# Kernel optimization log

Measured on AMD Instinct MI355X. Metric: run time of the kernel, lower is better.

## Reference

```python
import jax, jax.numpy as jnp
import numpy as np

D_EMB, D_PROJ, N_HEADS, HIDDEN = 640, 256, 4, 128
HEAD_DIM = D_PROJ // N_HEADS
B = 65536
EPS = 1e-5


def setup_inputs() -> dict:
    key = jax.random.key(0)
    ks = jax.random.split(key, 14)
    def w(k, shape, fan_in):
        return (jax.random.normal(k, shape, jnp.float32) / np.sqrt(fan_in)).astype(jnp.float32)
    return {
        "global_diff": jax.random.normal(ks[0], (B, D_EMB), jnp.float32),
        "local_diff": jax.random.normal(ks[1], (B, D_EMB), jnp.float32),
        # global/local projections ([in, out] layout; math identical to torch Linear)
        "Wg": w(ks[2], (D_EMB, D_PROJ), D_EMB), "bg": jnp.zeros((D_PROJ,), jnp.float32),
        "Wl": w(ks[3], (D_EMB, D_PROJ), D_EMB), "bl": jnp.zeros((D_PROJ,), jnp.float32),
        # MultiheadAttention packed in-proj (q|k|v) and out-proj
        "W_in": w(ks[4], (D_PROJ, 3 * D_PROJ), D_PROJ), "b_in": jnp.zeros((3 * D_PROJ,), jnp.float32),
        "W_out": w(ks[5], (D_PROJ, D_PROJ), D_PROJ), "b_out": jnp.zeros((D_PROJ,), jnp.float32),
        # LayerNorm
        "gamma": jnp.ones((D_PROJ,), jnp.float32), "beta": jnp.zeros((D_PROJ,), jnp.float32),
        # MLP head
        "W1": w(ks[6], (D_PROJ, HIDDEN), D_PROJ), "b1": jnp.zeros((HIDDEN,), jnp.float32),
        "W2": w(ks[7], (HIDDEN, 1), HIDDEN), "b2": jnp.zeros((1,), jnp.float32),
    }


def reference(global_diff, local_diff, Wg, bg, Wl, bl, W_in, b_in, W_out, b_out,
              gamma, beta, W1, b1, W2, b2):
    # projections (eval mode: dropout inactive)
    g = global_diff @ Wg + bg              # [B, P] -- the single query token
    l = local_diff @ Wl + bl               # [B, P]
    kv = jnp.stack([g, l], axis=1)         # [B, 2, P]

    Wq, Wk, Wv = jnp.split(W_in, 3, axis=1)
    bq, bk, bv = jnp.split(b_in, 3)
    b = g.shape[0]
    q = (g @ Wq + bq).reshape(b, N_HEADS, HEAD_DIM)        # [B, H, d]
    k = (kv @ Wk + bk).reshape(b, 2, N_HEADS, HEAD_DIM)    # [B, 2, H, d]
    v = (kv @ Wv + bv).reshape(b, 2, N_HEADS, HEAD_DIM)

    scale = 1.0 / np.sqrt(HEAD_DIM)
    scores = jnp.einsum('bhd,bshd->bhs', q, k) * scale     # [B, H, 2]
    attn = jax.nn.softmax(scores, axis=-1)
    ctx = jnp.einsum('bhs,bshd->bhd', attn, v).reshape(b, D_PROJ)
    attended = ctx @ W_out + b_out                         # [B, P]

    # residual + LayerNorm (eps=1e-5, torch default)
    x = g + attended
    mu = jnp.mean(x, axis=-1, keepdims=True)
    var = jnp.mean(jnp.square(x - mu), axis=-1, keepdims=True)
    y = (x - mu) * jax.lax.rsqrt(var + EPS) * gamma + beta

    # MLP head: Linear -> exact GELU (torch default) -> Linear
    h = jax.nn.gelu(y @ W1 + b1, approximate=False)
    out = (h @ W2 + b2).squeeze(-1)                        # [B]
    return out
```

## Files before the change

### kernel.cpp

```cpp
#include <hip/hip_runtime.h>
#include <math.h>

typedef __attribute__((ext_vector_type(4))) float f32x4;
typedef __attribute__((ext_vector_type(8))) __bf16 bf16x8;

static constexpr int WG_OFF = 0;
static constexpr int WL_OFF = 163840;
static constexpr int WQ_OFF = 327680;
static constexpr int WK_OFF = 393216;
static constexpr int WV_OFF = 458752;
static constexpr int WO_OFF = 524288;
static constexpr int W1_OFF = 589824;
static constexpr int W_TOTAL = 622592;

__device__ __forceinline__ unsigned short f2bf(float f) {
  unsigned u = __builtin_bit_cast(unsigned, f);
  u += 0x7FFFu + ((u >> 16) & 1u);
  return (unsigned short)(u >> 16);
}

__device__ __forceinline__ f32x4 mfma16(bf16x8 a, bf16x8 b, f32x4 c) {
  return __builtin_amdgcn_mfma_f32_16x16x32_bf16(a, b, c, 0, 0, 0);
}
__device__ __forceinline__ f32x4 fzero4() {
  f32x4 v; v[0] = 0.f; v[1] = 0.f; v[2] = 0.f; v[3] = 0.f; return v;
}

__device__ __forceinline__ bf16x8 ldB(const unsigned short* __restrict__ ws, int fragIdx, int lane) {
  return *(const bf16x8*)(ws + (size_t)(fragIdx * 64 + lane) * 8);
}

template <int STRIDE>
__device__ __forceinline__ bf16x8 ldA(const char* s, int row, int kbyte) {
  return *(const bf16x8*)(s + row * STRIDE + (kbyte ^ ((row & 7) << 4)));
}

__device__ __forceinline__ bf16x8 cvt8(float4 a, float4 b) {
  bf16x8 t;
  t[0] = (__bf16)a.x; t[1] = (__bf16)a.y; t[2] = (__bf16)a.z; t[3] = (__bf16)a.w;
  t[4] = (__bf16)b.x; t[5] = (__bf16)b.y; t[6] = (__bf16)b.z; t[7] = (__bf16)b.w;
  return t;
}

template <int N>
__device__ __forceinline__ void red16(float* v) {
#pragma unroll
  for (int m = 1; m < 16; m <<= 1) {
#pragma unroll
    for (int i = 0; i < N; ++i) v[i] += __shfl_xor(v[i], m);
  }
}

__device__ __forceinline__ void stageA32(const float* __restrict__ A, char* sA, int tid) {
#pragma unroll
  for (int i = 0; i < 5; ++i) {
    const int idx = i * 512 + tid;
    const int row = idx / 80;
    const int c8 = idx - row * 80;
    const float* ap = A + (size_t)idx * 8;
    float4 f0 = *(const float4*)ap;
    float4 f1 = *(const float4*)(ap + 4);
    *(bf16x8*)(sA + row * 1280 + ((c8 * 16) ^ ((row & 7) << 4))) = cvt8(f0, f1);
  }
}

__device__ __forceinline__ void proj640(const char* sA, const unsigned short* __restrict__ wsW,
                                        const float* __restrict__ bias, char* sDst,
                                        int f0, int lane) {
  const int l15 = lane & 15, kg4 = lane >> 4;
  f32x4 acc[2][2];
#pragma unroll
  for (int m = 0; m < 2; ++m)
#pragma unroll
    for (int n = 0; n < 2; ++n) acc[m][n] = fzero4();
  bf16x8 bp[4][2];
#pragma unroll
  for (int p = 0; p < 4; ++p) {
    bp[p][0] = ldB(wsW, p * 16 + f0, lane);
    bp[p][1] = ldB(wsW, p * 16 + f0 + 1, lane);
  }
#pragma unroll
  for (int kt = 0; kt < 20; ++kt) {
    bf16x8 b0 = bp[kt & 3][0], b1 = bp[kt & 3][1];
    if (kt < 16) {
      bp[kt & 3][0] = ldB(wsW, (kt + 4) * 16 + f0, lane);
      bp[kt & 3][1] = ldB(wsW, (kt + 4) * 16 + f0 + 1, lane);
    }
    const int kb = kt * 64 + kg4 * 16;
#pragma unroll
    for (int m = 0; m < 2; ++m) {
      bf16x8 a = ldA<1280>(sA, m * 16 + l15, kb);
      acc[m][0] = mfma16(a, b0, acc[m][0]);
      acc[m][1] = mfma16(a, b1, acc[m][1]);
    }
  }
#pragma unroll
  for (int n = 0; n < 2; ++n) {
    const int col = (f0 + n) * 16 + l15;
    const float bv = bias[col];
#pragma unroll
    for (int m = 0; m < 2; ++m)
#pragma unroll
      for (int r = 0; r < 4; ++r) {
        const int row = m * 16 + kg4 * 4 + r;
        *(__bf16*)(sDst + row * 512 + ((col * 2) ^ ((row & 7) << 4))) =
            (__bf16)(acc[m][n][r] + bv);
      }
  }
}

__device__ __forceinline__ void gemm256(const char* sA, const unsigned short* __restrict__ wsW,
                                        int f0, f32x4 (&acc)[2][2], int lane) {
  const int l15 = lane & 15, kg4 = lane >> 4;
#pragma unroll
  for (int kt = 0; kt < 8; ++kt) {
    bf16x8 b0 = ldB(wsW, kt * 16 + f0, lane);
    bf16x8 b1 = ldB(wsW, kt * 16 + f0 + 1, lane);
    const int kb = kt * 64 + kg4 * 16;
#pragma unroll
    for (int m = 0; m < 2; ++m) {
      bf16x8 a = ldA<512>(sA, m * 16 + l15, kb);
      acc[m][0] = mfma16(a, b0, acc[m][0]);
      acc[m][1] = mfma16(a, b1, acc[m][1]);
    }
  }
}

__device__ __forceinline__ void gemm256d(const char* sG, const char* sL,
                                         const unsigned short* __restrict__ wsW, int f0,
                                         f32x4 (&ag)[2][2], f32x4 (&al)[2][2], int lane) {
  const int l15 = lane & 15, kg4 = lane >> 4;
#pragma unroll
  for (int kt = 0; kt < 8; ++kt) {
    bf16x8 b0 = ldB(wsW, kt * 16 + f0, lane);
    bf16x8 b1 = ldB(wsW, kt * 16 + f0 + 1, lane);
    const int kb = kt * 64 + kg4 * 16;
#pragma unroll
    for (int m = 0; m < 2; ++m) {
      bf16x8 g = ldA<512>(sG, m * 16 + l15, kb);
      bf16x8 l = ldA<512>(sL, m * 16 + l15, kb);
      ag[m][0] = mfma16(g, b0, ag[m][0]);
      ag[m][1] = mfma16(g, b1, ag[m][1]);
      al[m][0] = mfma16(l, b0, al[m][0]);
      al[m][1] = mfma16(l, b1, al[m][1]);
    }
  }
}

__global__ void convert_w(const float* __restrict__ Wg, const float* __restrict__ Wl,
                          const float* __restrict__ Win, const float* __restrict__ Wout,
                          const float* __restrict__ W1, unsigned short* __restrict__ ws) {
  const int tid = blockIdx.x * 256 + threadIdx.x;
  if (tid >= W_TOTAL) return;
  const float* src;
  int stride, coloff, base, lognf;
  if (tid < WL_OFF)      { src = Wg;   stride = 256; coloff = 0;   base = WG_OFF; lognf = 4; }
  else if (tid < WQ_OFF) { src = Wl;   stride = 256; coloff = 0;   base = WL_OFF; lognf = 4; }
  else if (tid < WK_OFF) { src = Win;  stride = 768; coloff = 0;   base = WQ_OFF; lognf = 4; }
  else if (tid < WV_OFF) { src = Win;  stride = 768; coloff = 256; base = WK_OFF; lognf = 4; }
  else if (tid < WO_OFF) { src = Win;  stride = 768; coloff = 512; base = WV_OFF; lognf = 4; }
  else if (tid < W1_OFF) { src = Wout; stride = 256; coloff = 0;   base = WO_OFF; lognf = 4; }
  else                   { src = W1;   stride = 128; coloff = 0;   base = W1_OFF; lognf = 3; }
  const int idx = tid - base;
  const int j = idx & 7;
  const int lane = (idx >> 3) & 63;
  const int fl = idx >> 9;
  const int n = fl & ((1 << lognf) - 1);
  const int kt = fl >> lognf;
  const int k = kt * 32 + (lane >> 4) * 8 + j;
  const int col = coloff + n * 16 + (lane & 15);
  ws[tid] = f2bf(src[k * stride + col]);
}

__global__ __launch_bounds__(512, 4) void dca_fused(
    const float* __restrict__ gdiff, const float* __restrict__ ldiff,
    const float* __restrict__ bg, const float* __restrict__ bl,
    const float* __restrict__ bin, const float* __restrict__ bout,
    const float* __restrict__ gamma, const float* __restrict__ beta,
    const float* __restrict__ b1, const float* __restrict__ W2,
    const float* __restrict__ b2, const unsigned short* __restrict__ wsw,
    float* __restrict__ out) {
  __shared__ __align__(16) char sMem[73728];
  char* sA = sMem;
  char* sG = sMem + 40960;
  char* sL = sMem + 57344;
  float* sSc = (float*)sMem;
  float* sLN = (float*)(sMem + 2048);
  float* sMu = (float*)(sMem + 4096);
  float* sPO = (float*)(sMem + 4352);
  char* sY = sMem + 8192;

  const int tid = threadIdx.x;
  const int blk = blockIdx.x;
  const int lane = tid & 63, l15 = lane & 15, kg4 = lane >> 4;
  const int w = tid >> 6;
  const int f0 = w * 2;

  stageA32(gdiff + (size_t)blk * 32 * 640, sA, tid);
  __syncthreads();
  proj640(sA, wsw + WG_OFF, bg, sG, f0, lane);
  __syncthreads();
  stageA32(ldiff + (size_t)blk * 32 * 640, sA, tid);
  __syncthreads();
  proj640(sA, wsw + WL_OFF, bl, sL, f0, lane);
  __syncthreads();

  f32x4 q[2][2];
#pragma unroll
  for (int m = 0; m < 2; ++m)
#pragma unroll
    for (int n = 0; n < 2; ++n) q[m][n] = fzero4();
  gemm256(sG, wsw + WQ_OFF, f0, q, lane);
#pragma unroll
  for (int n = 0; n < 2; ++n) {
    const float bv = bin[(f0 + n) * 16 + l15];
#pragma unroll
    for (int m = 0; m < 2; ++m)
#pragma unroll
      for (int r = 0; r < 4; ++r) q[m][n][r] += bv;
  }
  f32x4 kg[2][2], kl[2][2];
#pragma unroll
  for (int m = 0; m < 2; ++m)
#pragma unroll
    for (int n = 0; n < 2; ++n) { kg[m][n] = fzero4(); kl[m][n] = fzero4(); }
  gemm256d(sG, sL, wsw + WK_OFF, f0, kg, kl, lane);

  float s[16];
#pragma unroll
  for (int m = 0; m < 2; ++m)
#pragma unroll
    for (int r = 0; r < 4; ++r) {
      float t0 = 0.f, t1 = 0.f;
#pragma unroll
      for (int n = 0; n < 2; ++n) {
        t0 += q[m][n][r] * kg[m][n][r];
        t1 += q[m][n][r] * kl[m][n][r];
      }
      s[m * 4 + r] = t0;
      s[8 + m * 4 + r] = t1;
    }
  red16<16>(s);
  if (l15 < 2) {
#pragma unroll
    for (int r = 0; r < 4; ++r) {
      const int row = l15 * 16 + kg4 * 4 + r;
      sSc[(w * 32 + row) * 2 + 0] = s[l15 * 4 + r];
      sSc[(w * 32 + row) * 2 + 1] = s[8 + l15 * 4 + r];
    }
  }
  __syncthreads();
  float a0[2][4], a1[2][4];
  {
    const int pw = w ^ 1;
#pragma unroll
    for (int m = 0; m < 2; ++m)
#pragma unroll
      for (int r = 0; r < 4; ++r) {
        const int row = m * 16 + kg4 * 4 + r;
        const float t0 = s[m * 4 + r] + sSc[(pw * 32 + row) * 2 + 0];
        const float t1 = s[8 + m * 4 + r] + sSc[(pw * 32 + row) * 2 + 1];
        const float d = (t0 - t1) * 0.125f;
        const float t = 1.0f / (1.0f + expf(d));
        a1[m][r] = t;
        a0[m][r] = 1.0f - t;
      }
  }
  f32x4 vg[2][2], vl[2][2];
#pragma unroll
  for (int m = 0; m < 2; ++m)
#pragma unroll
    for (int n = 0; n < 2; ++n) { vg[m][n] = fzero4(); vl[m][n] = fzero4(); }
  gemm256d(sG, sL, wsw + WV_OFF, f0, vg, vl, lane);
  f32x4 ctx[2][2];
#pragma unroll
  for (int n = 0; n < 2; ++n) {
    const float bv = bin[512 + (f0 + n) * 16 + l15];
#pragma unroll
    for (int m = 0; m < 2; ++m)
#pragma unroll
      for (int r = 0; r < 4; ++r)
        ctx[m][n][r] = a0[m][r] * vg[m][n][r] + a1[m][r] * vl[m][n][r] + bv;
  }
  __syncthreads();
#pragma unroll
  for (int n = 0; n < 2; ++n) {
    const int col = (f0 + n) * 16 + l15;
#pragma unroll
    for (int m = 0; m < 2; ++m)
#pragma unroll
      for (int r = 0; r < 4; ++r) {
        const int row = m * 16 + kg4 * 4 + r;
        *(__bf16*)(sL + row * 512 + ((col * 2) ^ ((row & 7) << 4))) = (__bf16)ctx[m][n][r];
      }
  }
  __syncthreads();

  f32x4 at[2][2];
#pragma unroll
  for (int m = 0; m < 2; ++m)
#pragma unroll
    for (int n = 0; n < 2; ++n) at[m][n] = fzero4();
  gemm256(sL, wsw + WO_OFF, f0, at, lane);
  float st[16];
#pragma unroll
  for (int i = 0; i < 16; ++i) st[i] = 0.f;
#pragma unroll
  for (int n = 0; n < 2; ++n) {
    const int col = (f0 + n) * 16 + l15;
    const float bv = bout[col];
#pragma unroll
    for (int m = 0; m < 2; ++m)
#pragma unroll
      for (int r = 0; r < 4; ++r) {
        const int row = m * 16 + kg4 * 4 + r;
        const float g =
            (float)*(const __bf16*)(sG + row * 512 + ((col * 2) ^ ((row & 7) << 4)));
        const float x = at[m][n][r] + bv + g;
        at[m][n][r] = x;
        st[m * 4 + r] += x;
        st[8 + m * 4 + r] += x * x;
      }
  }
  red16<16>(st);
  if (l15 < 2) {
#pragma unroll
    for (int r = 0; r < 4; ++r) {
      const int row = l15 * 16 + kg4 * 4 + r;
      sLN[(w * 32 + row) * 2 + 0] = st[l15 * 4 + r];
      sLN[(w * 32 + row) * 2 + 1] = st[8 + l15 * 4 + r];
    }
  }
  __syncthreads();
  if (tid < 64) {
    const int row = tid >> 1, j = tid & 1;
    float v = 0.f;
#pragma unroll
    for (int ww = 0; ww < 8; ++ww) v += sLN[(ww * 32 + row) * 2 + j];
    sMu[row * 2 + j] = v;
  }
  __syncthreads();
  float mu[2][4], rs[2][4];
#pragma unroll
  for (int m = 0; m < 2; ++m)
#pragma unroll
    for (int r = 0; r < 4; ++r) {
      const int row = m * 16 + kg4 * 4 + r;
      const float m_ = sMu[row * 2 + 0] * (1.0f / 256.0f);
      const float var = sMu[row * 2 + 1] * (1.0f / 256.0f) - m_ * m_;
      mu[m][r] = m_;
      rs[m][r] = rsqrtf(var + 1e-5f);
    }
#pragma unroll
  for (int n = 0; n < 2; ++n) {
    const int col = (f0 + n) * 16 + l15;
    const float ga = gamma[col], be = beta[col];
#pragma unroll
    for (int m = 0; m < 2; ++m)
#pragma unroll
      for (int r = 0; r < 4; ++r) {
        const int row = m * 16 + kg4 * 4 + r;
        const float y = (at[m][n][r] - mu[m][r]) * rs[m][r] * ga + be;
        *(__bf16*)(sY + row * 512 + ((col * 2) ^ ((row & 7) << 4))) = (__bf16)y;
      }
  }
  __syncthreads();

  f32x4 ha[2];
  ha[0] = fzero4();
  ha[1] = fzero4();
#pragma unroll
  for (int kt = 0; kt < 8; ++kt) {
    bf16x8 b = ldB(wsw + W1_OFF, kt * 8 + w, lane);
    const int kb = kt * 64 + kg4 * 16;
#pragma unroll
    for (int m = 0; m < 2; ++m) {
      bf16x8 a = ldA<512>(sY, m * 16 + l15, kb);
      ha[m] = mfma16(a, b, ha[m]);
    }
  }
  {
    const int colh = w * 16 + l15;
    const float bv1 = b1[colh], w2v = W2[colh];
    float o[8];
#pragma unroll
    for (int m = 0; m < 2; ++m)
#pragma unroll
      for (int r = 0; r < 4; ++r) {
        float hv = ha[m][r] + bv1;
        hv = 0.5f * hv * (1.0f + erff(hv * 0.70710678118654752f));
        o[m * 4 + r] = hv * w2v;
      }
    red16<8>(o);
    if (l15 < 2) {
#pragma unroll
      for (int r = 0; r < 4; ++r)
        sPO[w * 32 + l15 * 16 + kg4 * 4 + r] = o[l15 * 4 + r];
    }
  }
  __syncthreads();
  if (tid < 32) {
    float acc = b2[0];
#pragma unroll
    for (int ww = 0; ww < 8; ++ww) acc += sPO[ww * 32 + tid];
    out[(size_t)blk * 32 + tid] = acc;
  }
}

extern "C" void kernel_launch(void* const* d_in, const int* in_sizes, int n_in,
                              void* d_out, int out_size, void* d_ws, size_t ws_size,
                              hipStream_t stream) {
  (void)in_sizes; (void)n_in; (void)out_size; (void)ws_size;
  const float* gdiff = (const float*)d_in[0];
  const float* ldiff = (const float*)d_in[1];
  const float* Wg    = (const float*)d_in[2];
  const float* bg    = (const float*)d_in[3];
  const float* Wl    = (const float*)d_in[4];
  const float* bl    = (const float*)d_in[5];
  const float* Win   = (const float*)d_in[6];
  const float* bin   = (const float*)d_in[7];
  const float* Wout  = (const float*)d_in[8];
  const float* bout  = (const float*)d_in[9];
  const float* gamma = (const float*)d_in[10];
  const float* beta  = (const float*)d_in[11];
  const float* W1    = (const float*)d_in[12];
  const float* b1    = (const float*)d_in[13];
  const float* W2    = (const float*)d_in[14];
  const float* b2    = (const float*)d_in[15];
  unsigned short* ws = (unsigned short*)d_ws;
  float* out = (float*)d_out;

  convert_w<<<dim3((W_TOTAL + 255) / 256), dim3(256), 0, stream>>>(Wg, Wl, Win, Wout, W1, ws);
  dca_fused<<<dim3(2048), dim3(512), 0, stream>>>(gdiff, ldiff, bg, bl, bin, bout, gamma,
                                                  beta, b1, W2, b2,
                                                  (const unsigned short*)ws, out);
}
```

Before: 236.7 us.

## Double rows per block and stream fp32 inputs directly into MFMA fragments

Each block now processes 64 rows instead of 32 (grid halved), doubling weight-fragment reuse per load. The fp32 input staging through LDS is removed: the 640-wide projections read global memory straight into registers and convert to bf16 per MFMA fragment, which frees shared memory and drops two barriers. The dual-stream K/V gemms are split into sequential calls to limit register pressure. Costs are larger accumulator arrays (higher VGPR use, possibly lower occupancy), uncoalesced strided global reads for A, and fewer blocks to spread across CUs.

```diff
diff --git a/kernel.cpp b/kernel.cpp
--- a/kernel.cpp
+++ b/kernel.cpp
@@ -30,9 +30,14 @@
   return *(const bf16x8*)(ws + (size_t)(fragIdx * 64 + lane) * 8);
 }
 
-template <int STRIDE>
 __device__ __forceinline__ bf16x8 ldA(const char* s, int row, int kbyte) {
-  return *(const bf16x8*)(s + row * STRIDE + (kbyte ^ ((row & 7) << 4)));
+  return *(const bf16x8*)(s + row * 512 + (kbyte ^ ((row & 7) << 4)));
+}
+__device__ __forceinline__ void stC(char* s, int row, int col, float v) {
+  *(__bf16*)(s + row * 512 + ((col * 2) ^ ((row & 7) << 4))) = (__bf16)v;
+}
+__device__ __forceinline__ float ldC(const char* s, int row, int col) {
+  return (float)*(const __bf16*)(s + row * 512 + ((col * 2) ^ ((row & 7) << 4)));
 }
 
 __device__ __forceinline__ bf16x8 cvt8(float4 a, float4 b) {
@@ -51,45 +56,22 @@
   }
 }
 
-__device__ __forceinline__ void stageA32(const float* __restrict__ A, char* sA, int tid) {
-#pragma unroll
-  for (int i = 0; i < 5; ++i) {
-    const int idx = i * 512 + tid;
-    const int row = idx / 80;
-    const int c8 = idx - row * 80;
-    const float* ap = A + (size_t)idx * 8;
-    float4 f0 = *(const float4*)ap;
-    float4 f1 = *(const float4*)(ap + 4);
-    *(bf16x8*)(sA + row * 1280 + ((c8 * 16) ^ ((row & 7) << 4))) = cvt8(f0, f1);
-  }
-}
-
-__device__ __forceinline__ void proj640(const char* sA, const unsigned short* __restrict__ wsW,
-                                        const float* __restrict__ bias, char* sDst,
-                                        int f0, int lane) {
+__device__ __forceinline__ void projA(const float* __restrict__ A,
+                                      const unsigned short* __restrict__ wsW,
+                                      const float* __restrict__ bias, char* sDst,
+                                      int f0, int lane) {
   const int l15 = lane & 15, kg4 = lane >> 4;
-  f32x4 acc[2][2];
-#pragma unroll
-  for (int m = 0; m < 2; ++m)
-#pragma unroll
-    for (int n = 0; n < 2; ++n) acc[m][n] = fzero4();
-  bf16x8 bp[4][2];
-#pragma unroll
-  for (int p = 0; p < 4; ++p) {
-    bp[p][0] = ldB(wsW, p * 16 + f0, lane);
-    bp[p][1] = ldB(wsW, p * 16 + f0 + 1, lane);
-  }
-#pragma unroll
+  f32x4 acc[4][2];
+#pragma unroll
+  for (int m = 0; m < 4; ++m) { acc[m][0] = fzero4(); acc[m][1] = fzero4(); }
+#pragma unroll 5
   for (int kt = 0; kt < 20; ++kt) {
-    bf16x8 b0 = bp[kt & 3][0], b1 = bp[kt & 3][1];
-    if (kt < 16) {
-      bp[kt & 3][0] = ldB(wsW, (kt + 4) * 16 + f0, lane);
-      bp[kt & 3][1] = ldB(wsW, (kt + 4) * 16 + f0 + 1, lane);
-    }
-    const int kb = kt * 64 + kg4 * 16;
-#pragma unroll
-    for (int m = 0; m < 2; ++m) {
-      bf16x8 a = ldA<1280>(sA, m * 16 + l15, kb);
+    bf16x8 b0 = ldB(wsW, kt * 16 + f0, lane);
+    bf16x8 b1 = ldB(wsW, kt * 16 + f0 + 1, lane);
+#pragma unroll
+    for (int m = 0; m < 4; ++m) {
+      const float* ap = A + (size_t)(m * 16 + l15) * 640 + kt * 32 + kg4 * 8;
+      bf16x8 a = cvt8(*(const float4*)ap, *(const float4*)(ap + 4));
       acc[m][0] = mfma16(a, b0, acc[m][0]);
       acc[m][1] = mfma16(a, b1, acc[m][1]);
     }
@@ -99,18 +81,15 @@
     const int col = (f0 + n) * 16 + l15;
     const float bv = bias[col];
 #pragma unroll
-    for (int m = 0; m < 2; ++m)
-#pragma unroll
-      for (int r = 0; r < 4; ++r) {
-        const int row = m * 16 + kg4 * 4 + r;
-        *(__bf16*)(sDst + row * 512 + ((col * 2) ^ ((row & 7) << 4))) =
-            (__bf16)(acc[m][n][r] + bv);
-      }
+    for (int m = 0; m < 4; ++m)
+#pragma unroll
+      for (int r = 0; r < 4; ++r)
+        stC(sDst, m * 16 + kg4 * 4 + r, col, acc[m][n][r] + bv);
   }
 }
 
 __device__ __forceinline__ void gemm256(const char* sA, const unsigned short* __restrict__ wsW,
-                                        int f0, f32x4 (&acc)[2][2], int lane) {
+                                        int f0, f32x4 (&acc)[4][2], int lane) {
   const int l15 = lane & 15, kg4 = lane >> 4;
 #pragma unroll
   for (int kt = 0; kt < 8; ++kt) {
@@ -118,31 +97,10 @@
     bf16x8 b1 = ldB(wsW, kt * 16 + f0 + 1, lane);
     const int kb = kt * 64 + kg4 * 16;
 #pragma unroll
-    for (int m = 0; m < 2; ++m) {
-      bf16x8 a = ldA<512>(sA, m * 16 + l15, kb);
+    for (int m = 0; m < 4; ++m) {
+      bf16x8 a = ldA(sA, m * 16 + l15, kb);
       acc[m][0] = mfma16(a, b0, acc[m][0]);
       acc[m][1] = mfma16(a, b1, acc[m][1]);
-    }
-  }
-}
-
-__device__ __forceinline__ void gemm256d(const char* sG, const char* sL,
-                                         const unsigned short* __restrict__ wsW, int f0,
-                                         f32x4 (&ag)[2][2], f32x4 (&al)[2][2], int lane) {
-  const int l15 = lane & 15, kg4 = lane >> 4;
-#pragma unroll
-  for (int kt = 0; kt < 8; ++kt) {
-    bf16x8 b0 = ldB(wsW, kt * 16 + f0, lane);
-    bf16x8 b1 = ldB(wsW, kt * 16 + f0 + 1, lane);
-    const int kb = kt * 64 + kg4 * 16;
-#pragma unroll
-    for (int m = 0; m < 2; ++m) {
-      bf16x8 g = ldA<512>(sG, m * 16 + l15, kb);
-      bf16x8 l = ldA<512>(sL, m * 16 + l15, kb);
-      ag[m][0] = mfma16(g, b0, ag[m][0]);
-      ag[m][1] = mfma16(g, b1, ag[m][1]);
-      al[m][0] = mfma16(l, b0, al[m][0]);
-      al[m][1] = mfma16(l, b1, al[m][1]);
     }
   }
 }
@@ -181,14 +139,12 @@
     const float* __restrict__ b2, const unsigned short* __restrict__ wsw,
     float* __restrict__ out) {
   __shared__ __align__(16) char sMem[73728];
-  char* sA = sMem;
-  char* sG = sMem + 40960;
-  char* sL = sMem + 57344;
-  float* sSc = (float*)sMem;
-  float* sLN = (float*)(sMem + 2048);
-  float* sMu = (float*)(sMem + 4096);
-  float* sPO = (float*)(sMem + 4352);
-  char* sY = sMem + 8192;
+  char* sG = sMem;
+  char* sL = sMem + 32768;
+  float* sSc = (float*)(sMem + 65536);
+  float* sLN = (float*)(sMem + 69632);
+  float* sMu = (float*)(sMem + 65536);
+  float* sPO = (float*)(sMem + 66560);
 
   const int tid = threadIdx.x;
   const int blk = blockIdx.x;
@@ -196,153 +152,145 @@
   const int w = tid >> 6;
   const int f0 = w * 2;
 
-  stageA32(gdiff + (size_t)blk * 32 * 640, sA, tid);
-  __syncthreads();
-  proj640(sA, wsw + WG_OFF, bg, sG, f0, lane);
-  __syncthreads();
-  stageA32(ldiff + (size_t)blk * 32 * 640, sA, tid);
-  __syncthreads();
-  proj640(sA, wsw + WL_OFF, bl, sL, f0, lane);
-  __syncthreads();
-
-  f32x4 q[2][2];
-#pragma unroll
-  for (int m = 0; m < 2; ++m)
-#pragma unroll
-    for (int n = 0; n < 2; ++n) q[m][n] = fzero4();
+  projA(gdiff + (size_t)blk * 64 * 640, wsw + WG_OFF, bg, sG, f0, lane);
+  projA(ldiff + (size_t)blk * 64 * 640, wsw + WL_OFF, bl, sL, f0, lane);
+  __syncthreads();
+
+  f32x4 q[4][2];
+#pragma unroll
+  for (int m = 0; m < 4; ++m) { q[m][0] = fzero4(); q[m][1] = fzero4(); }
   gemm256(sG, wsw + WQ_OFF, f0, q, lane);
 #pragma unroll
   for (int n = 0; n < 2; ++n) {
     const float bv = bin[(f0 + n) * 16 + l15];
 #pragma unroll
-    for (int m = 0; m < 2; ++m)
+    for (int m = 0; m < 4; ++m)
 #pragma unroll
       for (int r = 0; r < 4; ++r) q[m][n][r] += bv;
   }
-  f32x4 kg[2][2], kl[2][2];
-#pragma unroll
-  for (int m = 0; m < 2; ++m)
-#pragma unroll
-    for (int n = 0; n < 2; ++n) { kg[m][n] = fzero4(); kl[m][n] = fzero4(); }
-  gemm256d(sG, sL, wsw + WK_OFF, f0, kg, kl, lane);
-
-  float s[16];
-#pragma unroll
-  for (int m = 0; m < 2; ++m)
-#pragma unroll
-    for (int r = 0; r < 4; ++r) {
-      float t0 = 0.f, t1 = 0.f;
-#pragma unroll
-      for (int n = 0; n < 2; ++n) {
-        t0 += q[m][n][r] * kg[m][n][r];
-        t1 += q[m][n][r] * kl[m][n][r];
-      }
-      s[m * 4 + r] = t0;
-      s[8 + m * 4 + r] = t1;
-    }
-  red16<16>(s);
+  float s[32];
+  {
+    f32x4 kk[4][2];
+#pragma unroll
+    for (int m = 0; m < 4; ++m) { kk[m][0] = fzero4(); kk[m][1] = fzero4(); }
+    gemm256(sG, wsw + WK_OFF, f0, kk, lane);
+#pragma unroll
+    for (int m = 0; m < 4; ++m)
+#pragma unroll
+      for (int r = 0; r < 4; ++r)
+        s[m * 4 + r] = q[m][0][r] * kk[m][0][r] + q[m][1][r] * kk[m][1][r];
+#pragma unroll
+    for (int m = 0; m < 4; ++m) { kk[m][0] = fzero4(); kk[m][1] = fzero4(); }
+    gemm256(sL, wsw + WK_OFF, f0, kk, lane);
+#pragma unroll
+    for (int m = 0; m < 4; ++m)
+#pragma unroll
+      for (int r = 0; r < 4; ++r)
+        s[16 + m * 4 + r] = q[m][0][r] * kk[m][0][r] + q[m][1][r] * kk[m][1][r];
+  }
+  red16<32>(s);
   if (l15 < 2) {
 #pragma unroll
-    for (int r = 0; r < 4; ++r) {
-      const int row = l15 * 16 + kg4 * 4 + r;
-      sSc[(w * 32 + row) * 2 + 0] = s[l15 * 4 + r];
-      sSc[(w * 32 + row) * 2 + 1] = s[8 + l15 * 4 + r];
-    }
-  }
-  __syncthreads();
-  float a0[2][4], a1[2][4];
+    for (int m = 0; m < 4; ++m)
+#pragma unroll
+      for (int r = 0; r < 4; ++r)
+        sSc[(w * 64 + m * 16 + kg4 * 4 + r) * 2 + l15] = s[l15 * 16 + m * 4 + r];
+  }
+  __syncthreads();
+  float a0[4][4], a1[4][4];
   {
     const int pw = w ^ 1;
 #pragma unroll
-    for (int m = 0; m < 2; ++m)
+    for (int m = 0; m < 4; ++m)
 #pragma unroll
       for (int r = 0; r < 4; ++r) {
         const int row = m * 16 + kg4 * 4 + r;
-        const float t0 = s[m * 4 + r] + sSc[(pw * 32 + row) * 2 + 0];
-        const float t1 = s[8 + m * 4 + r] + sSc[(pw * 32 + row) * 2 + 1];
+        const float t0 = s[m * 4 + r] + sSc[(pw * 64 + row) * 2 + 0];
+        const float t1 = s[16 + m * 4 + r] + sSc[(pw * 64 + row) * 2 + 1];
         const float d = (t0 - t1) * 0.125f;
         const float t = 1.0f / (1.0f + expf(d));
         a1[m][r] = t;
         a0[m][r] = 1.0f - t;
       }
   }
-  f32x4 vg[2][2], vl[2][2];
-#pragma unroll
-  for (int m = 0; m < 2; ++m)
-#pragma unroll
-    for (int n = 0; n < 2; ++n) { vg[m][n] = fzero4(); vl[m][n] = fzero4(); }
-  gemm256d(sG, sL, wsw + WV_OFF, f0, vg, vl, lane);
-  f32x4 ctx[2][2];
-#pragma unroll
-  for (int n = 0; n < 2; ++n) {
-    const float bv = bin[512 + (f0 + n) * 16 + l15];
-#pragma unroll
-    for (int m = 0; m < 2; ++m)
-#pragma unroll
-      for (int r = 0; r < 4; ++r)
-        ctx[m][n][r] = a0[m][r] * vg[m][n][r] + a1[m][r] * vl[m][n][r] + bv;
+  f32x4 ctx[4][2];
+  {
+    f32x4 vv[4][2];
+#pragma unroll
+    for (int m = 0; m < 4; ++m) { vv[m][0] = fzero4(); vv[m][1] = fzero4(); }
+    gemm256(sG, wsw + WV_OFF, f0, vv, lane);
+#pragma unroll
+    for (int n = 0; n < 2; ++n)
+#pragma unroll
+      for (int m = 0; m < 4; ++m)
+#pragma unroll
+        for (int r = 0; r < 4; ++r) ctx[m][n][r] = a0[m][r] * vv[m][n][r];
+#pragma unroll
+    for (int m = 0; m < 4; ++m) { vv[m][0] = fzero4(); vv[m][1] = fzero4(); }
+    gemm256(sL, wsw + WV_OFF, f0, vv, lane);
+#pragma unroll
+    for (int n = 0; n < 2; ++n) {
+      const float bv = bin[512 + (f0 + n) * 16 + l15];
+#pragma unroll
+      for (int m = 0; m < 4; ++m)
+#pragma unroll
+        for (int r = 0; r < 4; ++r) ctx[m][n][r] += a1[m][r] * vv[m][n][r] + bv;
+    }
   }
   __syncthreads();
 #pragma unroll
   for (int n = 0; n < 2; ++n) {
     const int col = (f0 + n) * 16 + l15;
 #pragma unroll
-    for (int m = 0; m < 2; ++m)
+    for (int m = 0; m < 4; ++m)
+#pragma unroll
+      for (int r = 0; r < 4; ++r)
+        stC(sL, m * 16 + kg4 * 4 + r, col, ctx[m][n][r]);
+  }
+  __syncthreads();
+
+  f32x4 at[4][2];
+#pragma unroll
+  for (int m = 0; m < 4; ++m) { at[m][0] = fzero4(); at[m][1] = fzero4(); }
+  gemm256(sL, wsw + WO_OFF, f0, at, lane);
+  float st[32];
+#pragma unroll
+  for (int i = 0; i < 32; ++i) st[i] = 0.f;
+#pragma unroll
+  for (int n = 0; n < 2; ++n) {
+    const int col = (f0 + n) * 16 + l15;
+    const float bv = bout[col];
+#pragma unroll
+    for (int m = 0; m < 4; ++m)
 #pragma unroll
       for (int r = 0; r < 4; ++r) {
         const int row = m * 16 + kg4 * 4 + r;
-        *(__bf16*)(sL + row * 512 + ((col * 2) ^ ((row & 7) << 4))) = (__bf16)ctx[m][n][r];
-      }
-  }
-  __syncthreads();
-
-  f32x4 at[2][2];
-#pragma unroll
-  for (int m = 0; m < 2; ++m)
-#pragma unroll
-    for (int n = 0; n < 2; ++n) at[m][n] = fzero4();
-  gemm256(sL, wsw + WO_OFF, f0, at, lane);
-  float st[16];
-#pragma unroll
-  for (int i = 0; i < 16; ++i) st[i] = 0.f;
-#pragma unroll
-  for (int n = 0; n < 2; ++n) {
-    const int col = (f0 + n) * 16 + l15;
-    const float bv = bout[col];
-#pragma unroll
-    for (int m = 0; m < 2; ++m)
-#pragma unroll
-      for (int r = 0; r < 4; ++r) {
-        const int row = m * 16 + kg4 * 4 + r;
-        const float g =
-            (float)*(const __bf16*)(sG + row * 512 + ((col * 2) ^ ((row & 7) << 4)));
-        const float x = at[m][n][r] + bv + g;
+        const float x = at[m][n][r] + bv + ldC(sG, row, col);
         at[m][n][r] = x;
         st[m * 4 + r] += x;
-        st[8 + m * 4 + r] += x * x;
+        st[16 + m * 4 + r] += x * x;
       }
   }
-  red16<16>(st);
+  red16<32>(st);
   if (l15 < 2) {
 #pragma unroll
-    for (int r = 0; r < 4; ++r) {
-      const int row = l15 * 16 + kg4 * 4 + r;
-      sLN[(w * 32 + row) * 2 + 0] = st[l15 * 4 + r];
-      sLN[(w * 32 + row) * 2 + 1] = st[8 + l15 * 4 + r];
-    }
-  }
-  __syncthreads();
-  if (tid < 64) {
+    for (int m = 0; m < 4; ++m)
+#pragma unroll
+      for (int r = 0; r < 4; ++r)
+        sLN[(w * 64 + m * 16 + kg4 * 4 + r) * 2 + l15] = st[l15 * 16 + m * 4 + r];
+  }
+  __syncthreads();
+  if (tid < 128) {
     const int row = tid >> 1, j = tid & 1;
     float v = 0.f;
 #pragma unroll
-    for (int ww = 0; ww < 8; ++ww) v += sLN[(ww * 32 + row) * 2 + j];
+    for (int ww = 0; ww < 8; ++ww) v += sLN[(ww * 64 + row) * 2 + j];
     sMu[row * 2 + j] = v;
   }
   __syncthreads();
-  float mu[2][4], rs[2][4];
-#pragma unroll
-  for (int m = 0; m < 2; ++m)
+  float mu[4][4], rs[4][4];
+#pragma unroll
+  for (int m = 0; m < 4; ++m)
 #pragma unroll
     for (int r = 0; r < 4; ++r) {
       const int row = m * 16 + kg4 * 4 + r;
@@ -356,54 +304,55 @@
     const int col = (f0 + n) * 16 + l15;
     const float ga = gamma[col], be = beta[col];
 #pragma unroll
-    for (int m = 0; m < 2; ++m)
+    for (int m = 0; m < 4; ++m)
 #pragma unroll
       for (int r = 0; r < 4; ++r) {
         const int row = m * 16 + kg4 * 4 + r;
-        const float y = (at[m][n][r] - mu[m][r]) * rs[m][r] * ga + be;
-        *(__bf16*)(sY + row * 512 + ((col * 2) ^ ((row & 7) << 4))) = (__bf16)y;
+        stC(sL, row, col, (at[m][n][r] - mu[m][r]) * rs[m][r] * ga + be);
       }
   }
   __syncthreads();
 
-  f32x4 ha[2];
-  ha[0] = fzero4();
-  ha[1] = fzero4();
+  f32x4 ha[4];
+#pragma unroll
+  for (int m = 0; m < 4; ++m) ha[m] = fzero4();
 #pragma unroll
   for (int kt = 0; kt < 8; ++kt) {
     bf16x8 b = ldB(wsw + W1_OFF, kt * 8 + w, lane);
     const int kb = kt * 64 + kg4 * 16;
 #pragma unroll
-    for (int m = 0; m < 2; ++m) {
-      bf16x8 a = ldA<512>(sY, m * 16 + l15, kb);
+    for (int m = 0; m < 4; ++m) {
+      bf16x8 a = ldA(sL, m * 16 + l15, kb);
       ha[m] = mfma16(a, b, ha[m]);
     }
   }
   {
     const int colh = w * 16 + l15;
     const float bv1 = b1[colh], w2v = W2[colh];
-    float o[8];
-#pragma unroll
-    for (int m = 0; m < 2; ++m)
+    float o[16];
+#pragma unroll
+    for (int m = 0; m < 4; ++m)
 #pragma unroll
       for (int r = 0; r < 4; ++r) {
         float hv = ha[m][r] + bv1;
         hv = 0.5f * hv * (1.0f + erff(hv * 0.70710678118654752f));
         o[m * 4 + r] = hv * w2v;
       }
-    red16<8>(o);
-    if (l15 < 2) {
-#pragma unroll
-      for (int r = 0; r < 4; ++r)
-        sPO[w * 32 + l15 * 16 + kg4 * 4 + r] = o[l15 * 4 + r];
-    }
-  }
-  __syncthreads();
-  if (tid < 32) {
+    red16<16>(o);
+    if (l15 == 0) {
+#pragma unroll
+      for (int m = 0; m < 4; ++m)
+#pragma unroll
+        for (int r = 0; r < 4; ++r)
+          sPO[w * 64 + m * 16 + kg4 * 4 + r] = o[m * 4 + r];
+    }
+  }
+  __syncthreads();
+  if (tid < 64) {
     float acc = b2[0];
 #pragma unroll
-    for (int ww = 0; ww < 8; ++ww) acc += sPO[ww * 32 + tid];
-    out[(size_t)blk * 32 + tid] = acc;
+    for (int ww = 0; ww < 8; ++ww) acc += sPO[ww * 64 + tid];
+    out[(size_t)blk * 64 + tid] = acc;
   }
 }
 
@@ -431,7 +380,7 @@
   float* out = (float*)d_out;
 
   convert_w<<<dim3((W_TOTAL + 255) / 256), dim3(256), 0, stream>>>(Wg, Wl, Win, Wout, W1, ws);
-  dca_fused<<<dim3(2048), dim3(512), 0, stream>>>(gdiff, ldiff, bg, bl, bin, bout, gamma,
+  dca_fused<<<dim3(1024), dim3(512), 0, stream>>>(gdiff, ldiff, bg, bl, bin, bout, gamma,
                                                   beta, b1, W2, b2,
                                                   (const unsigned short*)ws, out);
 }
```

Result: slower. 593.3 us (+150.7%).
